# Kernel optimization log

Hardware: AMD Instinct MI355X
Metric: run time of the kernel (lower is better)

Reference implementation:

```python
import jax, jax.numpy as jnp
import numpy as np

THETA = 0.5
NEG_SLOPE = 0.2


def setup_inputs() -> dict:
    key = jax.random.key(0)
    k1, k2, k3, k4, k5 = jax.random.split(key, 5)
    B, N, K, E, F = 32, 50000, 32, 6, 3
    return {
        "x": jax.random.normal(k1, (B, N), dtype=jnp.float32),
        "node_embeddings": jax.random.normal(k2, (N, E), dtype=jnp.float32),
        "fc_weight": jax.random.normal(k3, (F, E), dtype=jnp.float32),
        "fc_bias": jax.random.normal(k4, (F,), dtype=jnp.float32),
        "neighbor_list": jax.random.randint(k5, (N, K), 0, N, dtype=jnp.int32),
    }


def reference(x, node_embeddings, fc_weight, fc_bias, neighbor_list):
    # e: (B, N, E) = broadcast-add of scalar feature x and node embeddings
    e = x[..., None] + node_embeddings[None, :, :]
    # f: (B, N, F) = LeakyReLU(e @ W^T + b)
    f = jax.nn.leaky_relu(jnp.einsum('bne,fe->bnf', e, fc_weight) + fc_bias,
                          negative_slope=NEG_SLOPE)
    # gather neighbor features: (B, N, K, F); negative indices wrap like torch
    f_nbr = f[:, neighbor_list]
    df = f[:, :, None, :] - f_nbr               # (B, N, K, F)
    w = jnp.exp(-(df * df).sum(-1) / (2.0 * THETA)).mean(0)  # (N, K)
    mask = (neighbor_list >= 0).astype(w.dtype)
    return w * mask
```

## Files before the change

### kernel.cpp

```cpp
#include <hip/hip_runtime.h>

#define NN 50000
#define BB 32
#define KK 32
#define TN 64

typedef __attribute__((ext_vector_type(2))) _Float16 half2_t;
typedef __attribute__((ext_vector_type(8))) _Float16 half8_t;

__global__ __launch_bounds__(256) void prep_kernel(
    const float* __restrict__ x,
    const float* __restrict__ emb,
    const float* __restrict__ W,
    const float* __restrict__ bias,
    half2_t* __restrict__ xT,
    half8_t* __restrict__ gh)
{
    __shared__ float xs[BB][TN + 1];

    const int n0 = blockIdx.x * TN;
    const int t  = threadIdx.x;

#pragma unroll
    for (int j = 0; j < 8; ++j) {
        int idx = j * 256 + t;
        int r = idx >> 6, c = idx & 63;
        int n = n0 + c;
        xs[r][c] = (n < NN) ? x[r * NN + n] : 0.f;
    }
    __syncthreads();

#pragma unroll
    for (int it = 0; it < 4; ++it) {
        int slot = it * 256 + t;
        int nl = slot >> 4, b2 = slot & 15;
        int n = n0 + nl;
        if (n < NN) {
            half2_t p;
            p.x = (_Float16)xs[2 * b2][nl];
            p.y = (_Float16)xs[2 * b2 + 1][nl];
            xT[n * 16 + b2] = p;
            if (b2 == 0) {
                float e[6];
#pragma unroll
                for (int q = 0; q < 6; ++q) e[q] = emb[n * 6 + q];
                half8_t gv;
#pragma unroll
                for (int j = 0; j < 3; ++j) {
                    float s = bias[j];
#pragma unroll
                    for (int q = 0; q < 6; ++q) s += e[q] * W[j * 6 + q];
                    gv[2 * j] = (_Float16)s;
                    gv[2 * j + 1] = (_Float16)s;
                }
                gv[6] = (_Float16)0.f; gv[7] = (_Float16)0.f;
                gh[n] = gv;
            }
        }
    }
}

__global__ __launch_bounds__(256) void gather_kernel(
    const half2_t* __restrict__ xT,
    const half8_t* __restrict__ gh,
    const float* __restrict__ W,
    const int* __restrict__ nbr,
    float* __restrict__ out)
{
    __shared__ int nbr_sh[KK];

    const int n = blockIdx.x;
    const int t = threadIdx.x;

    if (t < KK) nbr_sh[t] = nbr[n * KK + t];
    __syncthreads();

    half2_t ws2[3];
#pragma unroll
    for (int j = 0; j < 3; ++j) {
        float s = 0.f;
#pragma unroll
        for (int q = 0; q < 6; ++q) s += W[j * 6 + q];
        _Float16 h = (_Float16)s;
        ws2[j].x = h; ws2[j].y = h;
    }
    half2_t lk; lk.x = (_Float16)0.2f; lk.y = (_Float16)0.2f;

    const int lane = t & 63;
    const int wave = t >> 6;
    const int sub  = lane >> 4;
    const int b2   = lane & 15;
    const int kg   = wave * 4 + sub;

    half2_t xn2 = xT[n * 16 + b2];
    half8_t gn8 = gh[n];
    half2_t fn[3];
#pragma unroll
    for (int j = 0; j < 3; ++j) {
        half2_t g = __builtin_shufflevector(gn8, gn8, 0, 1);
        if (j == 1) g = __builtin_shufflevector(gn8, gn8, 2, 3);
        if (j == 2) g = __builtin_shufflevector(gn8, gn8, 4, 5);
        half2_t u = xn2 * ws2[j] + g;
        fn[j] = __builtin_elementwise_max(u, u * lk);
    }

#pragma unroll
    for (int i = 0; i < 2; ++i) {
        int k = kg + i * 16;
        int m = nbr_sh[k];
        int mc = (m < 0) ? 0 : m;
        half2_t xm2 = xT[mc * 16 + b2];
        half8_t gm8 = gh[mc];
        half2_t g0 = __builtin_shufflevector(gm8, gm8, 0, 1);
        half2_t g1 = __builtin_shufflevector(gm8, gm8, 2, 3);
        half2_t g2 = __builtin_shufflevector(gm8, gm8, 4, 5);

        half2_t acc; acc.x = (_Float16)0.f; acc.y = (_Float16)0.f;
        half2_t u, d;
        u = xm2 * ws2[0] + g0; u = __builtin_elementwise_max(u, u * lk);
        d = fn[0] - u; acc = d * d + acc;
        u = xm2 * ws2[1] + g1; u = __builtin_elementwise_max(u, u * lk);
        d = fn[1] - u; acc = d * d + acc;
        u = xm2 * ws2[2] + g2; u = __builtin_elementwise_max(u, u * lk);
        d = fn[2] - u; acc = d * d + acc;

        float v = __expf(-(float)acc.x) + __expf(-(float)acc.y);
        v += __shfl_down(v, 8, 16);
        v += __shfl_down(v, 4, 16);
        v += __shfl_down(v, 2, 16);
        v += __shfl_down(v, 1, 16);
        if (b2 == 0) out[n * KK + k] = (m < 0) ? 0.f : v * (1.0f / 32.0f);
    }
}

extern "C" void kernel_launch(void* const* d_in, const int* in_sizes, int n_in,
                              void* d_out, int out_size, void* d_ws, size_t ws_size,
                              hipStream_t stream) {
    const float* x    = (const float*)d_in[0];
    const float* emb  = (const float*)d_in[1];
    const float* W    = (const float*)d_in[2];
    const float* bias = (const float*)d_in[3];
    const int*   nbr  = (const int*)d_in[4];
    float* out = (float*)d_out;

    half2_t* xT = (half2_t*)d_ws;
    half8_t* gh = (half8_t*)((char*)d_ws + NN * 16 * sizeof(half2_t));

    prep_kernel<<<(NN + TN - 1) / TN, 256, 0, stream>>>(x, emb, W, bias, xT, gh);
    gather_kernel<<<NN, 256, 0, stream>>>(xT, gh, W, nbr, out);
}
```

Before: 121.4 us.

## Process eight nodes per block with 4-wide half vectors per lane in gather

The gather kernel now handles 8 nodes per 256-thread block instead of one. Each lane covers 4 batch entries as half4 instead of 2, so 8 lanes span the batch, and each group loops over 8 neighbors. This cuts the block count by a factor of 8, amortises the per-block neighbor load and weight setup, and widens the per-lane loads. It relies on NN being divisible by GN, and it shortens the shuffle reduction to three steps.

```diff
diff --git a/kernel.cpp b/kernel.cpp
--- a/kernel.cpp
+++ b/kernel.cpp
@@ -4,9 +4,21 @@
 #define BB 32
 #define KK 32
 #define TN 64
+#define GN 8
 
 typedef __attribute__((ext_vector_type(2))) _Float16 half2_t;
+typedef __attribute__((ext_vector_type(4))) _Float16 half4_t;
 typedef __attribute__((ext_vector_type(8))) _Float16 half8_t;
+
+__device__ __forceinline__ half4_t g_dup0(half8_t v) {
+    return __builtin_shufflevector(v, v, 0, 1, 0, 1);
+}
+__device__ __forceinline__ half4_t g_dup1(half8_t v) {
+    return __builtin_shufflevector(v, v, 2, 3, 2, 3);
+}
+__device__ __forceinline__ half4_t g_dup2(half8_t v) {
+    return __builtin_shufflevector(v, v, 4, 5, 4, 5);
+}
 
 __global__ __launch_bounds__(256) void prep_kernel(
     const float* __restrict__ x,
@@ -61,75 +73,81 @@
 }
 
 __global__ __launch_bounds__(256) void gather_kernel(
-    const half2_t* __restrict__ xT,
+    const half4_t* __restrict__ xT4,
     const half8_t* __restrict__ gh,
     const float* __restrict__ W,
     const int* __restrict__ nbr,
     float* __restrict__ out)
 {
-    __shared__ int nbr_sh[KK];
+    __shared__ int nbr_sh[GN * KK];
 
-    const int n = blockIdx.x;
-    const int t = threadIdx.x;
+    const int t  = threadIdx.x;
+    const int n0 = blockIdx.x * GN;
 
-    if (t < KK) nbr_sh[t] = nbr[n * KK + t];
+    nbr_sh[t] = nbr[n0 * KK + t];
     __syncthreads();
 
-    half2_t ws2[3];
+    half4_t ws4[3];
 #pragma unroll
     for (int j = 0; j < 3; ++j) {
         float s = 0.f;
 #pragma unroll
         for (int q = 0; q < 6; ++q) s += W[j * 6 + q];
         _Float16 h = (_Float16)s;
-        ws2[j].x = h; ws2[j].y = h;
+        ws4[j].x = h; ws4[j].y = h; ws4[j].z = h; ws4[j].w = h;
     }
-    half2_t lk; lk.x = (_Float16)0.2f; lk.y = (_Float16)0.2f;
+    half4_t lk;
+    lk.x = (_Float16)0.2f; lk.y = (_Float16)0.2f;
+    lk.z = (_Float16)0.2f; lk.w = (_Float16)0.2f;
 
-    const int lane = t & 63;
-    const int wave = t >> 6;
-    const int sub  = lane >> 4;
-    const int b2   = lane & 15;
-    const int kg   = wave * 4 + sub;
+    const int l  = t & 7;
+    const int sg = t >> 3;
+    const int nl = sg >> 2;
+    const int kg = (sg & 3) * 8;
+    const int n  = n0 + nl;
 
-    half2_t xn2 = xT[n * 16 + b2];
+    half4_t xn4 = xT4[n * 8 + l];
     half8_t gn8 = gh[n];
-    half2_t fn[3];
-#pragma unroll
-    for (int j = 0; j < 3; ++j) {
-        half2_t g = __builtin_shufflevector(gn8, gn8, 0, 1);
-        if (j == 1) g = __builtin_shufflevector(gn8, gn8, 2, 3);
-        if (j == 2) g = __builtin_shufflevector(gn8, gn8, 4, 5);
-        half2_t u = xn2 * ws2[j] + g;
-        fn[j] = __builtin_elementwise_max(u, u * lk);
+    half4_t fn[3];
+    {
+        half4_t u0 = xn4 * ws4[0] + g_dup0(gn8);
+        fn[0] = __builtin_elementwise_max(u0, u0 * lk);
+        half4_t u1 = xn4 * ws4[1] + g_dup1(gn8);
+        fn[1] = __builtin_elementwise_max(u1, u1 * lk);
+        half4_t u2 = xn4 * ws4[2] + g_dup2(gn8);
+        fn[2] = __builtin_elementwise_max(u2, u2 * lk);
     }
 
+    const int mbase = nl * KK + kg;
+
 #pragma unroll
-    for (int i = 0; i < 2; ++i) {
-        int k = kg + i * 16;
-        int m = nbr_sh[k];
-        int mc = (m < 0) ? 0 : m;
-        half2_t xm2 = xT[mc * 16 + b2];
+    for (int i = 0; i < 8; ++i) {
+        int m  = nbr_sh[mbase + i];
+        int mc = m > 0 ? m : 0;
+        half4_t xm4 = xT4[mc * 8 + l];
         half8_t gm8 = gh[mc];
-        half2_t g0 = __builtin_shufflevector(gm8, gm8, 0, 1);
-        half2_t g1 = __builtin_shufflevector(gm8, gm8, 2, 3);
-        half2_t g2 = __builtin_shufflevector(gm8, gm8, 4, 5);
 
-        half2_t acc; acc.x = (_Float16)0.f; acc.y = (_Float16)0.f;
-        half2_t u, d;
-        u = xm2 * ws2[0] + g0; u = __builtin_elementwise_max(u, u * lk);
-        d = fn[0] - u; acc = d * d + acc;
-        u = xm2 * ws2[1] + g1; u = __builtin_elementwise_max(u, u * lk);
-        d = fn[1] - u; acc = d * d + acc;
-        u = xm2 * ws2[2] + g2; u = __builtin_elementwise_max(u, u * lk);
-        d = fn[2] - u; acc = d * d + acc;
-
-        float v = __expf(-(float)acc.x) + __expf(-(float)acc.y);
-        v += __shfl_down(v, 8, 16);
-        v += __shfl_down(v, 4, 16);
-        v += __shfl_down(v, 2, 16);
-        v += __shfl_down(v, 1, 16);
-        if (b2 == 0) out[n * KK + k] = (m < 0) ? 0.f : v * (1.0f / 32.0f);
+        half4_t acc;
+        acc.x = (_Float16)0.f; acc.y = (_Float16)0.f;
+        acc.z = (_Float16)0.f; acc.w = (_Float16)0.f;
+        {
+            half4_t u, d;
+            u = xm4 * ws4[0] + g_dup0(gm8);
+            u = __builtin_elementwise_max(u, u * lk);
+            d = fn[0] - u; acc = d * d + acc;
+            u = xm4 * ws4[1] + g_dup1(gm8);
+            u = __builtin_elementwise_max(u, u * lk);
+            d = fn[1] - u; acc = d * d + acc;
+            u = xm4 * ws4[2] + g_dup2(gm8);
+            u = __builtin_elementwise_max(u, u * lk);
+            d = fn[2] - u; acc = d * d + acc;
+        }
+        float v = (__expf(-(float)acc.x) + __expf(-(float)acc.y))
+                + (__expf(-(float)acc.z) + __expf(-(float)acc.w));
+        v += __shfl_down(v, 4, 8);
+        v += __shfl_down(v, 2, 8);
+        v += __shfl_down(v, 1, 8);
+        if (l == 0) out[n * KK + kg + i] = (m < 0) ? 0.f : v * (1.0f / 32.0f);
     }
 }
 
@@ -147,5 +165,5 @@
     half8_t* gh = (half8_t*)((char*)d_ws + NN * 16 * sizeof(half2_t));
 
     prep_kernel<<<(NN + TN - 1) / TN, 256, 0, stream>>>(x, emb, W, bias, xT, gh);
-    gather_kernel<<<NN, 256, 0, stream>>>(xT, gh, W, nbr, out);
+    gather_kernel<<<NN / GN, 256, 0, stream>>>((const half4_t*)xT, gh, W, nbr, out);
 }
```

Measured after the change: 99.26 us. 1.22x faster.
